# Kernel optimization log

Hardware: AMD Instinct MI355X
Metric: run time of the kernel (lower is better)

Reference implementation:

```python
import jax, jax.numpy as jnp
import numpy as np
from jax import lax

NPOINT = 1024
NSAMPLE = 32
RADIUS = 0.2
ALPHA = 0.2  # leaky relu slope


def fps(xyz, npoint):
    """Farthest point sampling. xyz: (B,N,3) -> idx (B,npoint) int32."""
    B, N, _ = xyz.shape
    first = jnp.zeros((B,), dtype=jnp.int32)
    dist0 = jnp.full((B, N), 1e10, dtype=xyz.dtype)

    def step(carry, _):
        dist, last = carry
        lp = jnp.take_along_axis(xyz, last[:, None, None], axis=1)  # (B,1,3)
        nd = jnp.sum((xyz - lp) ** 2, axis=-1)                      # (B,N)
        dist = jnp.minimum(dist, nd)
        nxt = jnp.argmax(dist, axis=-1).astype(jnp.int32)
        return (dist, nxt), nxt

    (_, _), idxs = lax.scan(step, (dist0, first), None, length=npoint - 1)
    return jnp.concatenate([first[:, None], idxs.T], axis=1)  # (B,npoint)


def ball_query(xyz, new_xyz, radius, nsample):
    """First-nsample-in-index-order neighbors within radius. -> idx (B,n,k) int32."""
    B, N, _ = xyz.shape
    d2 = (jnp.sum(new_xyz ** 2, -1)[:, :, None]
          + jnp.sum(xyz ** 2, -1)[:, None, :]
          - 2.0 * jnp.einsum('bnc,bmc->bnm', new_xyz, xyz))  # (B,n,N)
    mask = d2 <= radius * radius
    cand = jnp.where(mask, jnp.arange(N, dtype=jnp.int32)[None, None, :], N)
    srt = jnp.sort(cand, axis=-1)[..., :nsample]             # (B,n,k)
    first = srt[..., :1]
    idx = jnp.where(srt == N, first, srt)                     # pad with first valid
    return jnp.minimum(idx, N - 1).astype(jnp.int32)


def feature_enhance(g, f, gn, fn):
    """g(B,n,3) f(B,n,D) gn(B,n,k,3) fn(B,n,k,D) -> (B,n,k,3*3+1+(D+3)*3+1)."""
    # cal_feature_dis: scale neighbor xyz by exp(-mean |f - fn|)
    d = jnp.abs(f[:, :, None, :] - fn)                        # (B,n,k,D)
    fdist = jnp.exp(-jnp.mean(d, axis=-1, keepdims=True))     # (B,n,k,1)
    gn = gn * fdist                                           # broadcast == torch.repeat
    # avg_g: append softmax-geometry residual to features
    gmean = jnp.mean(gn, axis=2)                              # (B,n,3)
    gd = jnp.abs(jax.nn.softmax(gmean, -1) - jax.nn.softmax(g, -1))  # (B,n,3)
    gd = jnp.broadcast_to(gd[:, :, None, :], fn.shape[:3] + (3,))    # (B,n,k,3)
    fn = jnp.concatenate([fn, gd], axis=-1)                   # (B,n,k,D+3)
    f = jnp.concatenate([f, g], axis=-1)                      # (B,n,D+3)
    pg = jnp.broadcast_to(g[:, :, None, :], gn.shape)
    pf = jnp.broadcast_to(f[:, :, None, :], fn.shape)
    pg1 = pg - gn
    pf1 = pf - fn
    dg = jnp.sqrt(jnp.sum(pg1 ** 2, axis=-1, keepdims=True))
    df = jnp.sqrt(jnp.sum(pf1 ** 2, axis=-1, keepdims=True))
    pg2 = jnp.concatenate([gn, pg, pg1, dg], axis=-1)         # (B,n,k,10)
    pf2 = jnp.concatenate([fn, pf, pf1, df], axis=-1)         # (B,n,k,3(D+3)+1)
    return jnp.concatenate([pg2, pf2], axis=-1)


def hetero_attention(nfn, a, w1, b1):
    """Attention pooling over neighbors. nfn (B,n,k,nc) -> (B,n,c).
    (In the original, dgf->Conv2d 'disf' is computed but never used; omitted.)
    Dropout skipped (eval mode)."""
    e = jax.nn.leaky_relu(jnp.einsum('bnkc,cd->bnkd', nfn, a), ALPHA)
    attn = jax.nn.softmax(e, axis=2)                          # over k (dim=2)
    pooled = jnp.sum(attn * nfn, axis=2)                      # (B,n,nc)
    return jnp.einsum('bnc,oc->bno', pooled, w1) + b1         # 1x1 Conv1d


def setup_inputs() -> dict:
    key = jax.random.key(0)
    k1, k2, k3, k4 = jax.random.split(key, 4)
    B, N, D = 8, 4096, 64
    nc, c_out = 212, 128  # nc = 3*3+1 + 3*(D+3)+1
    xyz = jax.random.uniform(k1, (B, N, 3), dtype=jnp.float32)
    features = jax.random.normal(k2, (B, D, N), dtype=jnp.float32)
    xav = 1.414 * np.sqrt(6.0 / (nc + nc))
    a = jax.random.uniform(k3, (nc, nc), minval=-xav, maxval=xav, dtype=jnp.float32)
    w1 = jax.random.normal(k4, (c_out, nc), dtype=jnp.float32) / np.sqrt(nc)
    b1 = jnp.zeros((c_out,), dtype=jnp.float32)
    return {"xyz": xyz, "features": features, "a": a, "w1": w1, "b1": b1}


def reference(xyz, features, a, w1, b1):
    B, N, _ = xyz.shape
    feat = jnp.transpose(features, (0, 2, 1))                 # (B,N,D)
    fps_idx = fps(xyz, NPOINT)                                # (B,n)
    bidx = jnp.arange(B)[:, None]
    new_xyz = xyz[bidx, fps_idx]                              # (B,n,3)
    f = feat[bidx, fps_idx]                                   # (B,n,D)
    nb_idx = ball_query(xyz, new_xyz, RADIUS, NSAMPLE)        # (B,n,k)
    bidx2 = jnp.arange(B)[:, None, None]
    gn = xyz[bidx2, nb_idx]                                   # (B,n,k,3)
    fn = feat[bidx2, nb_idx]                                  # (B,n,k,D)
    nfn = feature_enhance(new_xyz, f, gn, fn)                 # (B,n,k,212)
    new_features = hetero_attention(nfn, a, w1, b1)           # (B,n,c)
    return new_xyz, jnp.transpose(new_features, (0, 2, 1))    # (B,c,n)
```

## Files before the change

kernel.cpp:

```cpp
#include <hip/hip_runtime.h>
#include <hip/hip_bf16.h>

#define B_    8
#define N_    4096
#define D_    64
#define NP_   1024
#define K_    32
#define NC_   212
#define CO_   128
#define FPS_T 256
#define SVW   72

__device__ __forceinline__ float f32add(float a, float b) { return __fadd_rn(a, b); }
__device__ __forceinline__ float f32sub(float a, float b) { return __fsub_rn(a, b); }
__device__ __forceinline__ float f32mul(float a, float b) { return __fmul_rn(a, b); }

__device__ __forceinline__ void waveArgmaxDpp(float& best, int& bidx) {
#define AMAX_STEP(CTRL)                                                                     \
    {                                                                                       \
        int _v = __builtin_amdgcn_update_dpp(__float_as_int(best), __float_as_int(best),    \
                                             (CTRL), 0xf, 0xf, false);                      \
        int _i = __builtin_amdgcn_update_dpp(bidx, bidx, (CTRL), 0xf, 0xf, false);          \
        float _f = __int_as_float(_v);                                                      \
        if (_f > best || (_f == best && _i < bidx)) { best = _f; bidx = _i; }               \
    }
    AMAX_STEP(0x111);
    AMAX_STEP(0x112);
    AMAX_STEP(0x114);
    AMAX_STEP(0x118);
    AMAX_STEP(0x142);
    AMAX_STEP(0x143);
#undef AMAX_STEP
    best = __int_as_float(__builtin_amdgcn_readlane(__float_as_int(best), 63));
    bidx = __builtin_amdgcn_readlane(bidx, 63);
}

__global__ __launch_bounds__(FPS_T, 1) void fps_kernel(
    const float* __restrict__ xyz,
    int* __restrict__ fpsIdx, float* __restrict__ out0) {
    int b = blockIdx.x;
    const float* P = xyz + (size_t)b * N_ * 3;
    __shared__ float X[N_], Y[N_], Z[N_];
    __shared__ int   hist[NP_];
    __shared__ float redV[2][FPS_T / 64];
    __shared__ int   redI[2][FPS_T / 64];
    int tid = threadIdx.x;
    for (int i = tid; i < N_; i += FPS_T) {
        X[i] = P[i * 3 + 0];
        Y[i] = P[i * 3 + 1];
        Z[i] = P[i * 3 + 2];
    }
    if (tid == 0) hist[0] = 0;
    __syncthreads();

    const int PPT = N_ / FPS_T;
    float px[PPT], py[PPT], pz[PPT], dist[PPT];
#pragma unroll
    for (int c = 0; c < PPT; c++) {
        int j = tid + FPS_T * c;
        px[c] = X[j]; py[c] = Y[j]; pz[c] = Z[j];
        dist[c] = 1e10f;
    }
    int last = 0;
    for (int it = 1; it < NP_; ++it) {
        float lx = X[last], ly = Y[last], lz = Z[last];
        float best = -1.0f; int bidx = 0;
#pragma unroll
        for (int c = 0; c < PPT; c++) {
            float dx = f32sub(px[c], lx), dy = f32sub(py[c], ly), dz = f32sub(pz[c], lz);
            float nd = f32add(f32add(f32mul(dx, dx), f32mul(dy, dy)), f32mul(dz, dz));
            float d  = fminf(dist[c], nd);
            dist[c] = d;
            if (d > best) { best = d; bidx = tid + FPS_T * c; }
        }
        waveArgmaxDpp(best, bidx);
        int par = it & 1;
        if ((tid & 63) == 0) { redV[par][tid >> 6] = best; redI[par][tid >> 6] = bidx; }
        __syncthreads();
        float bv = redV[par][0]; int bi = redI[par][0];
#pragma unroll
        for (int w = 1; w < FPS_T / 64; w++) {
            float ov = redV[par][w]; int oi = redI[par][w];
            if (ov > bv || (ov == bv && oi < bi)) { bv = ov; bi = oi; }
        }
        last = bi;
        if (tid == 0) hist[it] = last;
    }
    __syncthreads();
    for (int i = tid; i < NP_; i += FPS_T) {
        int j = hist[i];
        fpsIdx[b * NP_ + i] = j;
        size_t o = (size_t)(b * NP_ + i) * 3;
        out0[o + 0] = X[j]; out0[o + 1] = Y[j]; out0[o + 2] = Z[j];
    }
}

__global__ __launch_bounds__(256) void fused_kernel(
    const float* __restrict__ feat, const float* __restrict__ xyz,
    const float* __restrict__ newxyz, const int* __restrict__ fpsIdx,
    const float* __restrict__ A, const float* __restrict__ W1,
    const float* __restrict__ B1, float* __restrict__ out1) {
    int q = blockIdx.x;
    int b = q >> 10, n = q & (NP_ - 1);
    int tid = threadIdx.x;
    __shared__ float sV[K_][SVW];
    __shared__ float sF[68];
    __shared__ float sFD[K_];
    __shared__ float sGD[3];
    __shared__ float sGsum[3];
    __shared__ float sPool[NC_];
    __shared__ int   sNb[K_];
    __shared__ int   sCnt;

    if (tid < D_) sF[tid] = feat[((size_t)b * D_ + tid) * N_ + fpsIdx[q]];
    if (tid >= D_ && tid < D_ + 3) sF[tid] = newxyz[q * 3 + (tid - D_)];

    if (tid < 64) {
        int lane = tid;
        if (lane < K_) sNb[lane] = N_ - 1;
        const float* P = xyz + (size_t)b * N_ * 3;
        float qx = newxyz[q * 3 + 0];
        float qy = newxyz[q * 3 + 1];
        float qz = newxyz[q * 3 + 2];
        float sq = f32add(f32add(f32mul(qx, qx), f32mul(qy, qy)), f32mul(qz, qz));
        const float R2 = (float)(0.2 * 0.2);
        int count = 0;
        for (int base = 0; base < N_ && count < K_; base += 64) {
            int j = base + lane;
            float x = P[j * 3 + 0];
            float y = P[j * 3 + 1];
            float z = P[j * 3 + 2];
            float sxj = f32add(f32add(f32mul(x, x), f32mul(y, y)), f32mul(z, z));
            float dot = __fmaf_rn(qz, z, __fmaf_rn(qy, y, __fmul_rn(qx, x)));
            float d2  = f32sub(f32add(sq, sxj), f32mul(2.0f, dot));
            bool in = (d2 <= R2);
            unsigned long long m = __ballot(in);
            if (in) {
                int pos = count + __popcll(m & ((1ull << lane) - 1ull));
                if (pos < K_) sNb[pos] = j;
            }
            count += __popcll(m);
        }
        if (lane == 0) sCnt = (count < K_) ? count : K_;
    }
    __syncthreads();
    int cnt = sCnt;

    {
        int k = tid >> 3, l = tid & 7;
        int j = (k < cnt || cnt == 0) ? sNb[k] : sNb[0];
        const float* src = feat + (size_t)b * D_ * N_ + j;
#pragma unroll
        for (int dd = 0; dd < 8; dd++) {
            int d = l * 8 + dd;
            sV[k][4 + d] = src[(size_t)d * N_];
        }
    }
    if (tid < 96) {
        int k = tid / 3, c = tid % 3;
        int j = (k < cnt || cnt == 0) ? sNb[k] : sNb[0];
        sV[k][c] = xyz[((size_t)b * N_ + j) * 3 + c];
        sV[k][69 + c] = 0.f;
    }
    __syncthreads();

    {
        int k = tid >> 3, ds = (tid & 7) * 8;
        float s = 0.f;
#pragma unroll
        for (int j = 0; j < 8; j++) s += fabsf(sF[ds + j] - sV[k][4 + ds + j]);
        s += __shfl_xor(s, 1); s += __shfl_xor(s, 2); s += __shfl_xor(s, 4);
        if ((tid & 7) == 0) sFD[k] = __expf(-s * (1.0f / 64.0f));
    }
    __syncthreads();

    if (tid < 96) {
        int k = tid / 3, c = tid % 3;
        sV[k][c] = sV[k][c] * sFD[k];
    }
    __syncthreads();

    if (tid < K_) {
        int k = tid;
        float a0 = sF[64] - sV[k][0], a1 = sF[65] - sV[k][1], a2 = sF[66] - sV[k][2];
        sV[k][3] = sqrtf(a0 * a0 + a1 * a1 + a2 * a2);
    }
    if (tid >= 64 && tid < 67) {
        int c = tid - 64;
        float s = 0.f;
        for (int k = 0; k < K_; k++) s += sV[k][c];
        sGsum[c] = s;
    }
    __syncthreads();

    if (tid == 0) {
        float m0 = sGsum[0] * (1.f / K_), m1 = sGsum[1] * (1.f / K_), m2 = sGsum[2] * (1.f / K_);
        float mm = fmaxf(m0, fmaxf(m1, m2));
        float e0 = __expf(m0 - mm), e1 = __expf(m1 - mm), e2 = __expf(m2 - mm);
        float inv = 1.f / (e0 + e1 + e2);
        float g0 = sF[64], g1 = sF[65], g2 = sF[66];
        float gm = fmaxf(g0, fmaxf(g1, g2));
        float f0 = __expf(g0 - gm), f1 = __expf(g1 - gm), f2 = __expf(g2 - gm);
        float inv2 = 1.f / (f0 + f1 + f2);
        sGD[0] = fabsf(e0 * inv - f0 * inv2);
        sGD[1] = fabsf(e1 * inv - f1 * inv2);
        sGD[2] = fabsf(e2 * inv - f2 * inv2);
    }
    __syncthreads();

    {
        int k = tid >> 3, l = tid & 7;
        float s = 0.f;
        for (int c = l; c < 67; c += 8) {
            float v = (c < D_) ? (sF[c] - sV[k][4 + c]) : (sF[c] - sGD[c - D_]);
            s += v * v;
        }
        s += __shfl_xor(s, 1); s += __shfl_xor(s, 2); s += __shfl_xor(s, 4);
        if (l == 0) sV[k][68] = sqrtf(s);
    }
    __syncthreads();

    if (tid < NC_) {
        const float* Ac = A + tid;
        float g0 = sF[64], g1 = sF[65], g2 = sF[66];
        float base = 0.f;
        base += Ac[(size_t)3 * NC_] * g0 + Ac[(size_t)4 * NC_] * g1 + Ac[(size_t)5 * NC_] * g2;
#pragma unroll 4
        for (int i = 0; i < 67; i++) base += Ac[(size_t)(77 + i) * NC_] * sF[i];
#pragma unroll
        for (int j = 0; j < 3; j++) {
            float gdj = sGD[j], gj = sF[64 + j];
            base += Ac[(size_t)(74 + j) * NC_] * gdj + Ac[(size_t)(208 + j) * NC_] * (gj - gdj);
        }
#pragma unroll 4
        for (int i = 0; i < D_; i++) base += Ac[(size_t)(144 + i) * NC_] * sF[i];

        float acc[K_];
#pragma unroll
        for (int k = 0; k < K_; k++) acc[k] = 0.f;

        {
            float q0 = Ac[0] - Ac[(size_t)6 * NC_];
            float q1 = Ac[(size_t)1 * NC_] - Ac[(size_t)7 * NC_];
            float q2 = Ac[(size_t)2 * NC_] - Ac[(size_t)8 * NC_];
            float q3 = Ac[(size_t)9 * NC_];
#pragma unroll
            for (int k = 0; k < K_; k++) {
                float4 v = *(const float4*)&sV[k][0];
                acc[k] = fmaf(v.x, q0, fmaf(v.y, q1, fmaf(v.z, q2, fmaf(v.w, q3, acc[k]))));
            }
        }
        for (int gi = 0; gi < 16; gi++) {
            int i0 = gi * 4;
            float q0 = Ac[(size_t)(10 + i0 + 0) * NC_] - Ac[(size_t)(144 + i0 + 0) * NC_];
            float q1 = Ac[(size_t)(10 + i0 + 1) * NC_] - Ac[(size_t)(144 + i0 + 1) * NC_];
            float q2 = Ac[(size_t)(10 + i0 + 2) * NC_] - Ac[(size_t)(144 + i0 + 2) * NC_];
            float q3 = Ac[(size_t)(10 + i0 + 3) * NC_] - Ac[(size_t)(144 + i0 + 3) * NC_];
#pragma unroll
            for (int k = 0; k < K_; k++) {
                float4 v = *(const float4*)&sV[k][4 + i0];
                acc[k] = fmaf(v.x, q0, fmaf(v.y, q1, fmaf(v.z, q2, fmaf(v.w, q3, acc[k]))));
            }
        }
        {
            float q0 = Ac[(size_t)211 * NC_];
#pragma unroll
            for (int k = 0; k < K_; k++) acc[k] = fmaf(sV[k][68], q0, acc[k]);
        }

        float m = -1e30f;
#pragma unroll
        for (int k = 0; k < K_; k++) {
            float v = base + acc[k];
            v = (v > 0.f) ? v : 0.2f * v;
            acc[k] = v;
            m = fmaxf(m, v);
        }
        float ssum = 0.f;
#pragma unroll
        for (int k = 0; k < K_; k++) { float e = __expf(acc[k] - m); acc[k] = e; ssum += e; }
        float inv = 1.f / ssum;

        int col; float addv; float sgn;
        if      (tid < 3)   { col = tid;       addv = 0.f;           sgn = 1.f; }
        else if (tid < 6)   { col = 0;         addv = sF[61 + tid];  sgn = 0.f; }
        else if (tid < 9)   { col = tid - 6;   addv = sF[58 + tid];  sgn = -1.f; }
        else if (tid == 9)  { col = 3;         addv = 0.f;           sgn = 1.f; }
        else if (tid < 74)  { col = tid - 6;   addv = 0.f;           sgn = 1.f; }
        else if (tid < 77)  { col = 0;         addv = sGD[tid - 74]; sgn = 0.f; }
        else if (tid < 144) { col = 0;         addv = sF[tid - 77];  sgn = 0.f; }
        else if (tid < 208) { col = tid - 140; addv = sF[tid - 144]; sgn = -1.f; }
        else if (tid < 211) { col = 0;         addv = sF[tid - 144] - sGD[tid - 208]; sgn = 0.f; }
        else                { col = 68;        addv = 0.f;           sgn = 1.f; }
        float s = 0.f;
#pragma unroll
        for (int k = 0; k < K_; k++) s += acc[k] * sV[k][col];
        sPool[tid] = addv + sgn * (s * inv);
    }
    __syncthreads();

    if (tid < CO_) {
        const float* w = W1 + (size_t)tid * NC_;
        float accO = 0.f;
        for (int c = 0; c < NC_; c += 4) {
            float4 wv = *(const float4*)(w + c);
            accO += wv.x * sPool[c] + wv.y * sPool[c + 1] + wv.z * sPool[c + 2] + wv.w * sPool[c + 3];
        }
        accO += B1[tid];
        out1[((size_t)b * CO_ + tid) * NP_ + n] = accO;
    }
}

extern "C" void kernel_launch(void* const* d_in, const int* in_sizes, int n_in,
                              void* d_out, int out_size, void* d_ws, size_t ws_size,
                              hipStream_t stream) {
    (void)in_sizes; (void)n_in; (void)out_size; (void)ws_size;
    const float* xyz      = (const float*)d_in[0];
    const float* features = (const float*)d_in[1];
    const float* A        = (const float*)d_in[2];
    const float* W1       = (const float*)d_in[3];
    const float* B1       = (const float*)d_in[4];
    float* out0 = (float*)d_out;
    float* out1 = out0 + (size_t)B_ * NP_ * 3;

    int* fpsIdx = (int*)d_ws;

    fps_kernel<<<dim3(B_), dim3(FPS_T), 0, stream>>>(xyz, fpsIdx, out0);
    fused_kernel<<<dim3(B_ * NP_), dim3(256), 0, stream>>>(features, xyz, out0, fpsIdx,
                                                           A, W1, B1, out1);
}
```

Measured before the change: 1.297 ms.

## Merge FPS and grouping kernels into one persistent kernel with progress flags

Combines farthest point sampling and the per-query fused grouping/attention work into a single launch. Block roles come from an atomic ticket, so the first eight blocks run FPS and publish sampled indices in chunks of 16 through release-stored progress counters. Consumer blocks spin on those counters and start their queries as soon as their index is ready, overlapping the serial FPS with the heavy downstream work. This hides much of the FPS latency, but spinning blocks occupy CU slots, the extra memset adds a small cost, and the FPS blocks may be slowed by sharing CUs with consumer blocks.

```diff
diff --git a/kernel.cpp b/kernel.cpp
--- a/kernel.cpp
+++ b/kernel.cpp
@@ -8,8 +8,8 @@
 #define K_    32
 #define NC_   212
 #define CO_   128
-#define FPS_T 256
 #define SVW   72
+#define PUB   16
 
 __device__ __forceinline__ float f32add(float a, float b) { return __fadd_rn(a, b); }
 __device__ __forceinline__ float f32sub(float a, float b) { return __fsub_rn(a, b); }
@@ -24,46 +24,55 @@
         float _f = __int_as_float(_v);                                                      \
         if (_f > best || (_f == best && _i < bidx)) { best = _f; bidx = _i; }               \
     }
-    AMAX_STEP(0x111);
-    AMAX_STEP(0x112);
-    AMAX_STEP(0x114);
-    AMAX_STEP(0x118);
-    AMAX_STEP(0x142);
-    AMAX_STEP(0x143);
+    AMAX_STEP(0x111); AMAX_STEP(0x112); AMAX_STEP(0x114);
+    AMAX_STEP(0x118); AMAX_STEP(0x142); AMAX_STEP(0x143);
 #undef AMAX_STEP
     best = __int_as_float(__builtin_amdgcn_readlane(__float_as_int(best), 63));
     bidx = __builtin_amdgcn_readlane(bidx, 63);
 }
 
-__global__ __launch_bounds__(FPS_T, 1) void fps_kernel(
-    const float* __restrict__ xyz,
-    int* __restrict__ fpsIdx, float* __restrict__ out0) {
-    int b = blockIdx.x;
+struct FpsSm {
+    float X[N_], Y[N_], Z[N_];
+    int   hist[NP_];
+    float redV[2][4];
+    int   redI[2][4];
+};
+struct FusedSm {
+    float sV[K_][SVW];
+    float sF[68];
+    float sFD[K_];
+    float sGD[3];
+    float sGsum[3];
+    float sPool[NC_];
+    int   sNb[K_];
+    int   sCnt;
+};
+union MegaSm { FpsSm f; FusedSm u; };
+
+__device__ __forceinline__ void fps_role(
+    int b, const float* __restrict__ xyz, int* fpsIdx, float* out0,
+    int* progress, FpsSm& sm) {
     const float* P = xyz + (size_t)b * N_ * 3;
-    __shared__ float X[N_], Y[N_], Z[N_];
-    __shared__ int   hist[NP_];
-    __shared__ float redV[2][FPS_T / 64];
-    __shared__ int   redI[2][FPS_T / 64];
     int tid = threadIdx.x;
-    for (int i = tid; i < N_; i += FPS_T) {
-        X[i] = P[i * 3 + 0];
-        Y[i] = P[i * 3 + 1];
-        Z[i] = P[i * 3 + 2];
-    }
-    if (tid == 0) hist[0] = 0;
-    __syncthreads();
-
-    const int PPT = N_ / FPS_T;
+    for (int i = tid; i < N_; i += 256) {
+        sm.X[i] = P[i * 3 + 0];
+        sm.Y[i] = P[i * 3 + 1];
+        sm.Z[i] = P[i * 3 + 2];
+    }
+    if (tid == 0) sm.hist[0] = 0;
+    __syncthreads();
+
+    const int PPT = N_ / 256;
     float px[PPT], py[PPT], pz[PPT], dist[PPT];
 #pragma unroll
     for (int c = 0; c < PPT; c++) {
-        int j = tid + FPS_T * c;
-        px[c] = X[j]; py[c] = Y[j]; pz[c] = Z[j];
+        int j = tid + 256 * c;
+        px[c] = sm.X[j]; py[c] = sm.Y[j]; pz[c] = sm.Z[j];
         dist[c] = 1e10f;
     }
     int last = 0;
     for (int it = 1; it < NP_; ++it) {
-        float lx = X[last], ly = Y[last], lz = Z[last];
+        float lx = sm.X[last], ly = sm.Y[last], lz = sm.Z[last];
         float best = -1.0f; int bidx = 0;
 #pragma unroll
         for (int c = 0; c < PPT; c++) {
@@ -71,57 +80,74 @@
             float nd = f32add(f32add(f32mul(dx, dx), f32mul(dy, dy)), f32mul(dz, dz));
             float d  = fminf(dist[c], nd);
             dist[c] = d;
-            if (d > best) { best = d; bidx = tid + FPS_T * c; }
+            if (d > best) { best = d; bidx = tid + 256 * c; }
         }
         waveArgmaxDpp(best, bidx);
         int par = it & 1;
-        if ((tid & 63) == 0) { redV[par][tid >> 6] = best; redI[par][tid >> 6] = bidx; }
+        if ((tid & 63) == 0) { sm.redV[par][tid >> 6] = best; sm.redI[par][tid >> 6] = bidx; }
         __syncthreads();
-        float bv = redV[par][0]; int bi = redI[par][0];
-#pragma unroll
-        for (int w = 1; w < FPS_T / 64; w++) {
-            float ov = redV[par][w]; int oi = redI[par][w];
+        float bv = sm.redV[par][0]; int bi = sm.redI[par][0];
+#pragma unroll
+        for (int w = 1; w < 4; w++) {
+            float ov = sm.redV[par][w]; int oi = sm.redI[par][w];
             if (ov > bv || (ov == bv && oi < bi)) { bv = ov; bi = oi; }
         }
         last = bi;
-        if (tid == 0) hist[it] = last;
-    }
-    __syncthreads();
-    for (int i = tid; i < NP_; i += FPS_T) {
-        int j = hist[i];
-        fpsIdx[b * NP_ + i] = j;
-        size_t o = (size_t)(b * NP_ + i) * 3;
-        out0[o + 0] = X[j]; out0[o + 1] = Y[j]; out0[o + 2] = Z[j];
-    }
-}
-
-__global__ __launch_bounds__(256) void fused_kernel(
-    const float* __restrict__ feat, const float* __restrict__ xyz,
-    const float* __restrict__ newxyz, const int* __restrict__ fpsIdx,
+        if (tid == 0) sm.hist[it] = last;
+
+        if ((it & (PUB - 1)) == 0) {
+            if (tid < PUB) {
+                int s = it - PUB + tid;
+                int j = sm.hist[s];
+                fpsIdx[b * NP_ + s] = j;
+                size_t o = (size_t)(b * NP_ + s) * 3;
+                out0[o + 0] = sm.X[j]; out0[o + 1] = sm.Y[j]; out0[o + 2] = sm.Z[j];
+            }
+            if (tid == 0) {
+                __threadfence();
+                __hip_atomic_store(&progress[b], it, __ATOMIC_RELEASE,
+                                   __HIP_MEMORY_SCOPE_AGENT);
+            }
+        }
+    }
+    __syncthreads();
+    if (tid < PUB) {
+        int s = NP_ - PUB + tid;
+        int j = sm.hist[s];
+        fpsIdx[b * NP_ + s] = j;
+        size_t o = (size_t)(b * NP_ + s) * 3;
+        out0[o + 0] = sm.X[j]; out0[o + 1] = sm.Y[j]; out0[o + 2] = sm.Z[j];
+    }
+    if (tid == 0) {
+        __threadfence();
+        __hip_atomic_store(&progress[b], NP_, __ATOMIC_RELEASE, __HIP_MEMORY_SCOPE_AGENT);
+    }
+}
+
+__device__ __forceinline__ void fused_role(
+    int q, const float* __restrict__ feat, const float* __restrict__ xyz,
+    const float* newxyz, const int* fpsIdx, int* progress,
     const float* __restrict__ A, const float* __restrict__ W1,
-    const float* __restrict__ B1, float* __restrict__ out1) {
-    int q = blockIdx.x;
+    const float* __restrict__ B1, float* __restrict__ out1, FusedSm& sm) {
     int b = q >> 10, n = q & (NP_ - 1);
     int tid = threadIdx.x;
-    __shared__ float sV[K_][SVW];
-    __shared__ float sF[68];
-    __shared__ float sFD[K_];
-    __shared__ float sGD[3];
-    __shared__ float sGsum[3];
-    __shared__ float sPool[NC_];
-    __shared__ int   sNb[K_];
-    __shared__ int   sCnt;
-
-    if (tid < D_) sF[tid] = feat[((size_t)b * D_ + tid) * N_ + fpsIdx[q]];
-    if (tid >= D_ && tid < D_ + 3) sF[tid] = newxyz[q * 3 + (tid - D_)];
+
+    while (__hip_atomic_load(&progress[b], __ATOMIC_ACQUIRE, __HIP_MEMORY_SCOPE_AGENT) <= n)
+        __builtin_amdgcn_s_sleep(32);
+    __syncthreads();
+
+    int   fj = __hip_atomic_load(&fpsIdx[q], __ATOMIC_RELAXED, __HIP_MEMORY_SCOPE_AGENT);
+    float qx = __hip_atomic_load(&newxyz[q * 3 + 0], __ATOMIC_RELAXED, __HIP_MEMORY_SCOPE_AGENT);
+    float qy = __hip_atomic_load(&newxyz[q * 3 + 1], __ATOMIC_RELAXED, __HIP_MEMORY_SCOPE_AGENT);
+    float qz = __hip_atomic_load(&newxyz[q * 3 + 2], __ATOMIC_RELAXED, __HIP_MEMORY_SCOPE_AGENT);
+
+    if (tid < D_) sm.sF[tid] = feat[((size_t)b * D_ + tid) * N_ + fj];
+    if (tid >= D_ && tid < D_ + 3) sm.sF[tid] = (tid == D_) ? qx : (tid == D_ + 1 ? qy : qz);
 
     if (tid < 64) {
         int lane = tid;
-        if (lane < K_) sNb[lane] = N_ - 1;
+        if (lane < K_) sm.sNb[lane] = N_ - 1;
         const float* P = xyz + (size_t)b * N_ * 3;
-        float qx = newxyz[q * 3 + 0];
-        float qy = newxyz[q * 3 + 1];
-        float qz = newxyz[q * 3 + 2];
         float sq = f32add(f32add(f32mul(qx, qx), f32mul(qy, qy)), f32mul(qz, qz));
         const float R2 = (float)(0.2 * 0.2);
         int count = 0;
@@ -137,30 +163,30 @@
             unsigned long long m = __ballot(in);
             if (in) {
                 int pos = count + __popcll(m & ((1ull << lane) - 1ull));
-                if (pos < K_) sNb[pos] = j;
+                if (pos < K_) sm.sNb[pos] = j;
             }
             count += __popcll(m);
         }
-        if (lane == 0) sCnt = (count < K_) ? count : K_;
-    }
-    __syncthreads();
-    int cnt = sCnt;
+        if (lane == 0) sm.sCnt = (count < K_) ? count : K_;
+    }
+    __syncthreads();
+    int cnt = sm.sCnt;
 
     {
         int k = tid >> 3, l = tid & 7;
-        int j = (k < cnt || cnt == 0) ? sNb[k] : sNb[0];
+        int j = (k < cnt || cnt == 0) ? sm.sNb[k] : sm.sNb[0];
         const float* src = feat + (size_t)b * D_ * N_ + j;
 #pragma unroll
         for (int dd = 0; dd < 8; dd++) {
             int d = l * 8 + dd;
-            sV[k][4 + d] = src[(size_t)d * N_];
+            sm.sV[k][4 + d] = src[(size_t)d * N_];
         }
     }
     if (tid < 96) {
         int k = tid / 3, c = tid % 3;
-        int j = (k < cnt || cnt == 0) ? sNb[k] : sNb[0];
-        sV[k][c] = xyz[((size_t)b * N_ + j) * 3 + c];
-        sV[k][69 + c] = 0.f;
+        int j = (k < cnt || cnt == 0) ? sm.sNb[k] : sm.sNb[0];
+        sm.sV[k][c] = xyz[((size_t)b * N_ + j) * 3 + c];
+        sm.sV[k][69 + c] = 0.f;
     }
     __syncthreads();
 
@@ -168,43 +194,43 @@
         int k = tid >> 3, ds = (tid & 7) * 8;
         float s = 0.f;
 #pragma unroll
-        for (int j = 0; j < 8; j++) s += fabsf(sF[ds + j] - sV[k][4 + ds + j]);
+        for (int j = 0; j < 8; j++) s += fabsf(sm.sF[ds + j] - sm.sV[k][4 + ds + j]);
         s += __shfl_xor(s, 1); s += __shfl_xor(s, 2); s += __shfl_xor(s, 4);
-        if ((tid & 7) == 0) sFD[k] = __expf(-s * (1.0f / 64.0f));
+        if ((tid & 7) == 0) sm.sFD[k] = __expf(-s * (1.0f / 64.0f));
     }
     __syncthreads();
 
     if (tid < 96) {
         int k = tid / 3, c = tid % 3;
-        sV[k][c] = sV[k][c] * sFD[k];
+        sm.sV[k][c] = sm.sV[k][c] * sm.sFD[k];
     }
     __syncthreads();
 
     if (tid < K_) {
         int k = tid;
-        float a0 = sF[64] - sV[k][0], a1 = sF[65] - sV[k][1], a2 = sF[66] - sV[k][2];
-        sV[k][3] = sqrtf(a0 * a0 + a1 * a1 + a2 * a2);
+        float a0 = sm.sF[64] - sm.sV[k][0], a1 = sm.sF[65] - sm.sV[k][1], a2 = sm.sF[66] - sm.sV[k][2];
+        sm.sV[k][3] = sqrtf(a0 * a0 + a1 * a1 + a2 * a2);
     }
     if (tid >= 64 && tid < 67) {
         int c = tid - 64;
         float s = 0.f;
-        for (int k = 0; k < K_; k++) s += sV[k][c];
-        sGsum[c] = s;
+        for (int k = 0; k < K_; k++) s += sm.sV[k][c];
+        sm.sGsum[c] = s;
     }
     __syncthreads();
 
     if (tid == 0) {
-        float m0 = sGsum[0] * (1.f / K_), m1 = sGsum[1] * (1.f / K_), m2 = sGsum[2] * (1.f / K_);
+        float m0 = sm.sGsum[0] * (1.f / K_), m1 = sm.sGsum[1] * (1.f / K_), m2 = sm.sGsum[2] * (1.f / K_);
         float mm = fmaxf(m0, fmaxf(m1, m2));
         float e0 = __expf(m0 - mm), e1 = __expf(m1 - mm), e2 = __expf(m2 - mm);
         float inv = 1.f / (e0 + e1 + e2);
-        float g0 = sF[64], g1 = sF[65], g2 = sF[66];
+        float g0 = sm.sF[64], g1 = sm.sF[65], g2 = sm.sF[66];
         float gm = fmaxf(g0, fmaxf(g1, g2));
         float f0 = __expf(g0 - gm), f1 = __expf(g1 - gm), f2 = __expf(g2 - gm);
         float inv2 = 1.f / (f0 + f1 + f2);
-        sGD[0] = fabsf(e0 * inv - f0 * inv2);
-        sGD[1] = fabsf(e1 * inv - f1 * inv2);
-        sGD[2] = fabsf(e2 * inv - f2 * inv2);
+        sm.sGD[0] = fabsf(e0 * inv - f0 * inv2);
+        sm.sGD[1] = fabsf(e1 * inv - f1 * inv2);
+        sm.sGD[2] = fabsf(e2 * inv - f2 * inv2);
     }
     __syncthreads();
 
@@ -212,28 +238,28 @@
         int k = tid >> 3, l = tid & 7;
         float s = 0.f;
         for (int c = l; c < 67; c += 8) {
-            float v = (c < D_) ? (sF[c] - sV[k][4 + c]) : (sF[c] - sGD[c - D_]);
+            float v = (c < D_) ? (sm.sF[c] - sm.sV[k][4 + c]) : (sm.sF[c] - sm.sGD[c - D_]);
             s += v * v;
         }
         s += __shfl_xor(s, 1); s += __shfl_xor(s, 2); s += __shfl_xor(s, 4);
-        if (l == 0) sV[k][68] = sqrtf(s);
+        if (l == 0) sm.sV[k][68] = sqrtf(s);
     }
     __syncthreads();
 
     if (tid < NC_) {
         const float* Ac = A + tid;
-        float g0 = sF[64], g1 = sF[65], g2 = sF[66];
+        float g0 = sm.sF[64], g1 = sm.sF[65], g2 = sm.sF[66];
         float base = 0.f;
         base += Ac[(size_t)3 * NC_] * g0 + Ac[(size_t)4 * NC_] * g1 + Ac[(size_t)5 * NC_] * g2;
 #pragma unroll 4
-        for (int i = 0; i < 67; i++) base += Ac[(size_t)(77 + i) * NC_] * sF[i];
+        for (int i = 0; i < 67; i++) base += Ac[(size_t)(77 + i) * NC_] * sm.sF[i];
 #pragma unroll
         for (int j = 0; j < 3; j++) {
-            float gdj = sGD[j], gj = sF[64 + j];
+            float gdj = sm.sGD[j], gj = sm.sF[64 + j];
             base += Ac[(size_t)(74 + j) * NC_] * gdj + Ac[(size_t)(208 + j) * NC_] * (gj - gdj);
         }
 #pragma unroll 4
-        for (int i = 0; i < D_; i++) base += Ac[(size_t)(144 + i) * NC_] * sF[i];
+        for (int i = 0; i < D_; i++) base += Ac[(size_t)(144 + i) * NC_] * sm.sF[i];
 
         float acc[K_];
 #pragma unroll
@@ -246,7 +272,7 @@
             float q3 = Ac[(size_t)9 * NC_];
 #pragma unroll
             for (int k = 0; k < K_; k++) {
-                float4 v = *(const float4*)&sV[k][0];
+                float4 v = *(const float4*)&sm.sV[k][0];
                 acc[k] = fmaf(v.x, q0, fmaf(v.y, q1, fmaf(v.z, q2, fmaf(v.w, q3, acc[k]))));
             }
         }
@@ -258,14 +284,14 @@
             float q3 = Ac[(size_t)(10 + i0 + 3) * NC_] - Ac[(size_t)(144 + i0 + 3) * NC_];
 #pragma unroll
             for (int k = 0; k < K_; k++) {
-                float4 v = *(const float4*)&sV[k][4 + i0];
+                float4 v = *(const float4*)&sm.sV[k][4 + i0];
                 acc[k] = fmaf(v.x, q0, fmaf(v.y, q1, fmaf(v.z, q2, fmaf(v.w, q3, acc[k]))));
             }
         }
         {
             float q0 = Ac[(size_t)211 * NC_];
 #pragma unroll
-            for (int k = 0; k < K_; k++) acc[k] = fmaf(sV[k][68], q0, acc[k]);
+            for (int k = 0; k < K_; k++) acc[k] = fmaf(sm.sV[k][68], q0, acc[k]);
         }
 
         float m = -1e30f;
@@ -282,20 +308,20 @@
         float inv = 1.f / ssum;
 
         int col; float addv; float sgn;
-        if      (tid < 3)   { col = tid;       addv = 0.f;           sgn = 1.f; }
-        else if (tid < 6)   { col = 0;         addv = sF[61 + tid];  sgn = 0.f; }
-        else if (tid < 9)   { col = tid - 6;   addv = sF[58 + tid];  sgn = -1.f; }
-        else if (tid == 9)  { col = 3;         addv = 0.f;           sgn = 1.f; }
-        else if (tid < 74)  { col = tid - 6;   addv = 0.f;           sgn = 1.f; }
-        else if (tid < 77)  { col = 0;         addv = sGD[tid - 74]; sgn = 0.f; }
-        else if (tid < 144) { col = 0;         addv = sF[tid - 77];  sgn = 0.f; }
-        else if (tid < 208) { col = tid - 140; addv = sF[tid - 144]; sgn = -1.f; }
-        else if (tid < 211) { col = 0;         addv = sF[tid - 144] - sGD[tid - 208]; sgn = 0.f; }
-        else                { col = 68;        addv = 0.f;           sgn = 1.f; }
+        if      (tid < 3)   { col = tid;       addv = 0.f;              sgn = 1.f; }
+        else if (tid < 6)   { col = 0;         addv = sm.sF[61 + tid];  sgn = 0.f; }
+        else if (tid < 9)   { col = tid - 6;   addv = sm.sF[58 + tid];  sgn = -1.f; }
+        else if (tid == 9)  { col = 3;         addv = 0.f;              sgn = 1.f; }
+        else if (tid < 74)  { col = tid - 6;   addv = 0.f;              sgn = 1.f; }
+        else if (tid < 77)  { col = 0;         addv = sm.sGD[tid - 74]; sgn = 0.f; }
+        else if (tid < 144) { col = 0;         addv = sm.sF[tid - 77];  sgn = 0.f; }
+        else if (tid < 208) { col = tid - 140; addv = sm.sF[tid - 144]; sgn = -1.f; }
+        else if (tid < 211) { col = 0;         addv = sm.sF[tid - 144] - sm.sGD[tid - 208]; sgn = 0.f; }
+        else                { col = 68;        addv = 0.f;              sgn = 1.f; }
         float s = 0.f;
 #pragma unroll
-        for (int k = 0; k < K_; k++) s += acc[k] * sV[k][col];
-        sPool[tid] = addv + sgn * (s * inv);
+        for (int k = 0; k < K_; k++) s += acc[k] * sm.sV[k][col];
+        sm.sPool[tid] = addv + sgn * (s * inv);
     }
     __syncthreads();
 
@@ -304,10 +330,31 @@
         float accO = 0.f;
         for (int c = 0; c < NC_; c += 4) {
             float4 wv = *(const float4*)(w + c);
-            accO += wv.x * sPool[c] + wv.y * sPool[c + 1] + wv.z * sPool[c + 2] + wv.w * sPool[c + 3];
+            accO += wv.x * sm.sPool[c] + wv.y * sm.sPool[c + 1] + wv.z * sm.sPool[c + 2] + wv.w * sm.sPool[c + 3];
         }
         accO += B1[tid];
         out1[((size_t)b * CO_ + tid) * NP_ + n] = accO;
+    }
+}
+
+__global__ __launch_bounds__(256) void mega_kernel(
+    const float* __restrict__ xyz, const float* __restrict__ feat,
+    const float* __restrict__ A, const float* __restrict__ W1,
+    const float* __restrict__ B1,
+    int* hdr, int* fpsIdx, float* out0, float* out1) {
+    __shared__ MegaSm sm;
+    __shared__ int sRole;
+    if (threadIdx.x == 0) sRole = atomicAdd(&hdr[0], 1);
+    __syncthreads();
+    int role = sRole;
+    int* progress = hdr + 1;
+
+    if (role < B_) {
+        __builtin_amdgcn_s_setprio(3);
+        fps_role(role, xyz, fpsIdx, out0, progress, sm.f);
+        __builtin_amdgcn_s_setprio(0);
+    } else {
+        fused_role(role - B_, feat, xyz, out0, fpsIdx, progress, A, W1, B1, out1, sm.u);
     }
 }
 
@@ -323,9 +370,10 @@
     float* out0 = (float*)d_out;
     float* out1 = out0 + (size_t)B_ * NP_ * 3;
 
-    int* fpsIdx = (int*)d_ws;
-
-    fps_kernel<<<dim3(B_), dim3(FPS_T), 0, stream>>>(xyz, fpsIdx, out0);
-    fused_kernel<<<dim3(B_ * NP_), dim3(256), 0, stream>>>(features, xyz, out0, fpsIdx,
-                                                           A, W1, B1, out1);
-}
+    int* hdr    = (int*)d_ws;
+    int* fpsIdx = hdr + 16;
+
+    hipMemsetAsync(d_ws, 0, 64, stream);
+    mega_kernel<<<dim3(B_ * NP_ + B_), dim3(256), 0, stream>>>(
+        xyz, features, A, W1, B1, hdr, fpsIdx, out0, out1);
+}
```

New measurement: 1.950 ms. +50.3%, slower.
